# Optimization experiments

Hardware: AMD Instinct MI355X
Metric: run time of the kernel (lower is better)

Reference implementation:

```python
import jax, jax.numpy as jnp
import numpy as np

HIDDEN = 2048
NUM_HEADS = 16
NUM_KV_HEADS = 8
HEAD_DIM = 128
EPS = 1e-6
ROPE_THETA = 10000.0
T = 2048
Q_SIZE = NUM_HEADS * HEAD_DIM          # 2048
KV_SIZE = NUM_KV_HEADS * HEAD_DIM      # 1024


def setup_inputs() -> dict:
    key = jax.random.key(0)
    k1, k2, k3, k4, k5 = jax.random.split(key, 5)
    positions = jnp.arange(T, dtype=jnp.int32)
    hidden_states = jax.random.normal(k1, (T, HIDDEN), dtype=jnp.float32)
    s = 0.02
    qkv_w = jax.random.normal(k2, (Q_SIZE + 2 * KV_SIZE, HIDDEN), dtype=jnp.float32) * s
    o_w = jax.random.normal(k3, (HIDDEN, Q_SIZE), dtype=jnp.float32) * s
    q_norm_w = jnp.ones((HEAD_DIM,), dtype=jnp.float32) + 0.1 * jax.random.normal(k4, (HEAD_DIM,), dtype=jnp.float32)
    k_norm_w = jnp.ones((HEAD_DIM,), dtype=jnp.float32) + 0.1 * jax.random.normal(k5, (HEAD_DIM,), dtype=jnp.float32)
    return {"positions": positions, "hidden_states": hidden_states,
            "qkv_w": qkv_w, "q_norm_w": q_norm_w, "k_norm_w": k_norm_w, "o_w": o_w}


def _rms_norm(x, w):
    # x: [T, H, D], normalize over last dim
    var = jnp.mean(x * x, axis=-1, keepdims=True)
    return x * jax.lax.rsqrt(var + EPS) * w


def _rope(x, positions):
    # neox-style rotary over full head_dim; x: [T, H, D]
    half = HEAD_DIM // 2
    inv_freq = 1.0 / (ROPE_THETA ** (jnp.arange(0, half, dtype=jnp.float32) / half))
    freqs = positions.astype(jnp.float32)[:, None] * inv_freq  # [T, D/2]
    cos = jnp.cos(freqs)[:, None, :]  # [T, 1, D/2]
    sin = jnp.sin(freqs)[:, None, :]
    x1, x2 = x[..., :half], x[..., half:]
    return jnp.concatenate([x1 * cos - x2 * sin, x2 * cos + x1 * sin], axis=-1)


def reference(positions, hidden_states, qkv_w, q_norm_w, k_norm_w, o_w):
    G = NUM_HEADS // NUM_KV_HEADS  # query groups per kv head
    scale = HEAD_DIM ** -0.5
    qkv = hidden_states @ qkv_w.T  # [T, Q+2KV]
    q, k, v = jnp.split(qkv, [Q_SIZE, Q_SIZE + KV_SIZE], axis=-1)
    q = q.reshape(T, NUM_HEADS, HEAD_DIM)
    k = k.reshape(T, NUM_KV_HEADS, HEAD_DIM)
    v = v.reshape(T, NUM_KV_HEADS, HEAD_DIM)
    # qkv_bias=False path -> per-head RMSNorm on q and k
    q = _rms_norm(q, q_norm_w)
    k = _rms_norm(k, k_norm_w)
    q = _rope(q, positions)
    k = _rope(k, positions)
    # GQA causal attention
    qg = q.reshape(T, NUM_KV_HEADS, G, HEAD_DIM)
    scores = jnp.einsum('qkgd,skd->kgqs', qg, k) * scale  # [KV, G, T, T]
    causal = positions[:, None] >= positions[None, :]  # [T, T]
    scores = jnp.where(causal, scores, jnp.finfo(scores.dtype).min)
    probs = jax.nn.softmax(scores, axis=-1)
    ctx = jnp.einsum('kgqs,skd->qkgd', probs, v)  # [T, KV, G, D]
    ctx = ctx.reshape(T, Q_SIZE)
    return ctx @ o_w.T  # [T, HIDDEN]
```

## Files before the change

### kernel.cpp

```cpp
#include <hip/hip_runtime.h>
#include <math.h>

#define T_SEQ     2048
#define HIDDEN_   2048
#define NUM_HEADS 16
#define NUM_KV    8
#define HEAD_DIM  128
#define Q_SIZE    2048
#define KV_SIZE   1024
#define QKV_N     4096
#define QK_N      3072
#define EPS_      1e-6f

typedef __attribute__((ext_vector_type(8))) short short8;
typedef __attribute__((ext_vector_type(4))) float floatx4;

__device__ __forceinline__ unsigned short f2bf(float f) {
    unsigned int u = __float_as_uint(f);
    u += 0x7fffu + ((u >> 16) & 1u);
    return (unsigned short)(u >> 16);
}
__device__ __forceinline__ float b2f(unsigned short u) {
    return __uint_as_float((unsigned int)u << 16);
}

__device__ __forceinline__ void stage16(const unsigned short* g, unsigned short* lds_base) {
    __builtin_amdgcn_global_load_lds(
        (const __attribute__((address_space(1))) unsigned int*)g,
        (__attribute__((address_space(3))) unsigned int*)lds_base, 16, 0, 0);
}

#define H4 (T_SEQ * HIDDEN_ / 4)
#define W4 (QKV_N * HIDDEN_ / 4)
#define O4 (Q_SIZE * HIDDEN_ / 4)

__global__ __launch_bounds__(256) void convert_all(
    const float* __restrict__ hidden, const float* __restrict__ qkv_w,
    const float* __restrict__ o_w, unsigned short* __restrict__ hbf,
    unsigned short* __restrict__ wbf, unsigned short* __restrict__ obf)
{
    int i = blockIdx.x * 256 + threadIdx.x;
    const float4* src;
    ushort4* dst;
    int j;
    if (i < H4)            { src = (const float4*)hidden; dst = (ushort4*)hbf; j = i; }
    else if (i < H4 + W4)  { src = (const float4*)qkv_w;  dst = (ushort4*)wbf; j = i - H4; }
    else                   { src = (const float4*)o_w;    dst = (ushort4*)obf; j = i - H4 - W4;
                             if (j >= O4) return; }
    float4 v = src[j];
    ushort4 o;
    o.x = f2bf(v.x); o.y = f2bf(v.y); o.z = f2bf(v.z); o.w = f2bf(v.w);
    dst[j] = o;
}

template<int MODE>
__global__ __launch_bounds__(1024, 8) void gemm_nt_bf16(
    const unsigned short* __restrict__ A, const unsigned short* __restrict__ B,
    float* __restrict__ C,
    unsigned short* __restrict__ Qb, unsigned short* __restrict__ Kb,
    unsigned short* __restrict__ Vt,
    const int* __restrict__ positions,
    const float* __restrict__ qw, const float* __restrict__ kw,
    int M, int N, int K)
{
    __shared__ unsigned short smem[32768];
    unsigned short* const As0 = smem;
    unsigned short* const Bs0 = smem + 16384;

    const int tid  = threadIdx.x;
    const int w    = tid >> 6;
    const int lane = tid & 63;
    const int colL = lane & 15;
    const int quad = lane >> 4;
    const int bm = blockIdx.y * 128;
    const int bn = blockIdx.x * 128;
    const int wr = w >> 2;
    const int wc = w & 3;
    const int wm = wr * 32;
    const int wn = wc * 32;

    floatx4 acc[2][2];
    #pragma unroll
    for (int i = 0; i < 2; ++i)
        #pragma unroll
        for (int j = 0; j < 2; ++j)
            acc[i][j] = (floatx4){0.f, 0.f, 0.f, 0.f};

    const int s_r  = tid >> 3;
    const int s_lc = (tid & 7) ^ (s_r & 7);

    auto stage_tile = [&](int buf, int k0) {
        stage16(A + (size_t)(bm + s_r) * K + k0 + s_lc * 8,
                As0 + buf * 8192 + tid * 8);
        stage16(B + (size_t)(bn + s_r) * K + k0 + s_lc * 8,
                Bs0 + buf * 8192 + tid * 8);
    };

    const int nt = K >> 6;
    stage_tile(0, 0);

    for (int t = 0; t < nt; ++t) {
        const int b = t & 1;
        if (t + 1 < nt) {
            stage_tile(b ^ 1, (t + 1) << 6);
            asm volatile("s_waitcnt vmcnt(2)" ::: "memory");
        } else {
            asm volatile("s_waitcnt vmcnt(0)" ::: "memory");
        }
        __builtin_amdgcn_s_barrier();
        __builtin_amdgcn_sched_barrier(0);

        const unsigned short* la = As0 + b * 8192;
        const unsigned short* lb = Bs0 + b * 8192;
        #pragma unroll
        for (int kk = 0; kk < 2; ++kk) {
            short8 af[2], bfv[2];
            #pragma unroll
            for (int i = 0; i < 2; ++i) {
                int ra = wm + i * 16 + colL;
                af[i]  = *(const short8*)&la[ra * 64 + (((kk * 4 + quad) ^ (ra & 7)) * 8)];
            }
            #pragma unroll
            for (int j = 0; j < 2; ++j) {
                int rb = wn + j * 16 + colL;
                bfv[j] = *(const short8*)&lb[rb * 64 + (((kk * 4 + quad) ^ (rb & 7)) * 8)];
            }
            #pragma unroll
            for (int i = 0; i < 2; ++i)
                #pragma unroll
                for (int j = 0; j < 2; ++j)
                    acc[i][j] = __builtin_amdgcn_mfma_f32_16x16x32_bf16(af[i], bfv[j], acc[i][j], 0, 0, 0);
        }
        __builtin_amdgcn_sched_barrier(0);
        asm volatile("" ::: "memory");
        __builtin_amdgcn_s_barrier();
    }

    if constexpr (MODE == 0) {
        #pragma unroll
        for (int i = 0; i < 2; ++i)
            #pragma unroll
            for (int j = 0; j < 2; ++j)
                #pragma unroll
                for (int rr = 0; rr < 4; ++rr) {
                    int row = bm + wm + i * 16 + quad * 4 + rr;
                    int cc2 = bn + wn + j * 16 + colL;
                    C[(size_t)row * N + cc2] = acc[i][j][rr];
                }
    } else {
        if (bn < QK_N) {
            __shared__ float sums[4][128];
            unsigned short* xnL = smem;

            float p[2][4];
            #pragma unroll
            for (int i = 0; i < 2; ++i)
                #pragma unroll
                for (int rr = 0; rr < 4; ++rr) {
                    float sv = 0.f;
                    #pragma unroll
                    for (int j = 0; j < 2; ++j)
                        sv = fmaf(acc[i][j][rr], acc[i][j][rr], sv);
                    p[i][rr] = sv;
                }
            #pragma unroll
            for (int off = 1; off < 16; off <<= 1)
                #pragma unroll
                for (int i = 0; i < 2; ++i)
                    #pragma unroll
                    for (int rr = 0; rr < 4; ++rr)
                        p[i][rr] += __shfl_xor(p[i][rr], off, 64);
            if (colL == 0) {
                #pragma unroll
                for (int i = 0; i < 2; ++i)
                    #pragma unroll
                    for (int rr = 0; rr < 4; ++rr)
                        sums[wc][wm + i * 16 + quad * 4 + rr] = p[i][rr];
            }
            __syncthreads();

            float inv_r[2][4];
            #pragma unroll
            for (int i = 0; i < 2; ++i)
                #pragma unroll
                for (int rr = 0; rr < 4; ++rr) {
                    int row = wm + i * 16 + quad * 4 + rr;
                    float tot = (sums[0][row] + sums[1][row]) + (sums[2][row] + sums[3][row]);
                    inv_r[i][rr] = rsqrtf(tot * (1.0f / HEAD_DIM) + EPS_);
                }

            const float* nw = (bn < Q_SIZE) ? qw : kw;
            float wv[2];
            #pragma unroll
            for (int j = 0; j < 2; ++j)
                wv[j] = nw[wn + j * 16 + colL];

            #pragma unroll
            for (int i = 0; i < 2; ++i)
                #pragma unroll
                for (int j = 0; j < 2; ++j) {
                    ushort4 pk;
                    pk.x = f2bf(acc[i][j][0] * inv_r[i][0] * wv[j]);
                    pk.y = f2bf(acc[i][j][1] * inv_r[i][1] * wv[j]);
                    pk.z = f2bf(acc[i][j][2] * inv_r[i][2] * wv[j]);
                    pk.w = f2bf(acc[i][j][3] * inv_r[i][3] * wv[j]);
                    int d = wn + j * 16 + colL;
                    *(ushort4*)&xnL[d * 132 + wm + i * 16 + quad * 4] = pk;
                }
            __syncthreads();
            {
                const int r = tid >> 3;
                const int oct = tid & 7;
                const float pos = (float)positions[bm + r];
                const bool is_q = (bn < Q_SIZE);
                const float l2r = 13.287712379549449f / 64.0f;
                const float sc = 0.08838834764831845f;
                unsigned short* rowp;
                if (is_q) rowp = Qb + (size_t)(bm + r) * Q_SIZE + (bn >> 7) * HEAD_DIM;
                else      rowp = Kb + ((size_t)((bn - Q_SIZE) >> 7) * T_SEQ + bm + r) * HEAD_DIM;

                #pragma unroll
                for (int f4 = 0; f4 < 8; f4 += 4) {
                    ushort4 lo, hi;
                    #pragma unroll
                    for (int e = 0; e < 4; ++e) {
                        int f = oct * 8 + f4 + e;
                        float x1 = b2f(xnL[f * 132 + r]);
                        float x2 = b2f(xnL[(f + 64) * 132 + r]);
                        float sv, cv;
                        __sincosf(pos * exp2f(-(float)f * l2r), &sv, &cv);
                        float olo = fmaf(x1, cv, -x2 * sv);
                        float ohi = fmaf(x2, cv,  x1 * sv);
                        if (is_q) { olo *= sc; ohi *= sc; }
                        ((unsigned short*)&lo)[e] = f2bf(olo);
                        ((unsigned short*)&hi)[e] = f2bf(ohi);
                    }
                    *(ushort4*)(rowp + oct * 8 + f4)      = lo;
                    *(ushort4*)(rowp + 64 + oct * 8 + f4) = hi;
                }
            }
        } else {
            const int kvh = (bn - QK_N) >> 7;
            #pragma unroll
            for (int i = 0; i < 2; ++i)
                #pragma unroll
                for (int j = 0; j < 2; ++j) {
                    int d = wn + j * 16 + colL;
                    int tok = bm + wm + i * 16 + quad * 4;
                    ushort4 o;
                    o.x = f2bf(acc[i][j][0]); o.y = f2bf(acc[i][j][1]);
                    o.z = f2bf(acc[i][j][2]); o.w = f2bf(acc[i][j][3]);
                    *(ushort4*)&Vt[((size_t)kvh * HEAD_DIM + d) * T_SEQ + tok] = o;
                }
        }
    }
}

#define BQ 64
#define BK 32

__global__ __launch_bounds__(256) void attn_mfma(
    const unsigned short* __restrict__ Qb, const unsigned short* __restrict__ Kb,
    const unsigned short* __restrict__ Vt, unsigned short* __restrict__ ctxb,
    float* __restrict__ partO, float* __restrict__ partL)
{
    const int h = blockIdx.y;
    int qt, ch;
    {
        int x = blockIdx.x;
        if (x < 16) { qt = 16 + x; ch = 0; }
        else {
            int p = (x - 16) >> 1;
            if (((x - 16) & 1) == 0) { qt = 15 - p; ch = 0; }
            else                     { qt = 31 - p; ch = 1; }
        }
    }
    const int nch = (qt >= 16) ? 2 : 1;
    const int units = (ch == 0) ? ((qt + 1 < 16) ? 2 * (qt + 1) : 32)
                                : (2 * (qt + 1) - 32);
    const int q0 = qt * BQ;
    const int kv = h >> 1;
    const int tid = threadIdx.x;
    const int w = tid >> 6;
    const int lane = tid & 63;
    const int col = lane & 15;
    const int quad = lane >> 4;

    __shared__ unsigned short Ks[2][32 * 128];
    __shared__ unsigned short Vs[2][144 * 32];
    __shared__ unsigned short Ps[4][16][40];

    {
        int x = tid * 2;
        unsigned short vv = (x < 32) ? (unsigned short)0x3F80 : (unsigned short)0;
        ushort2 o = {vv, vv};
        *(ushort2*)&Vs[0][128 * 32 + x] = o;
        *(ushort2*)&Vs[1][128 * 32 + x] = o;
    }
    asm volatile("s_waitcnt lgkmcnt(0)" ::: "memory");

    short8 qf[4];
    {
        const unsigned short* qp = Qb + (size_t)(q0 + w * 16 + col) * Q_SIZE + h * HEAD_DIM;
        #pragma unroll
        for (int c = 0; c < 4; ++c)
            qf[c] = *(const short8*)(qp + c * 32 + quad * 8);
    }

    const unsigned short* kg[2];
    const unsigned short* vg[2];
    #pragma unroll
    for (int it = 0; it < 2; ++it) {
        int s = it * 256 + tid;
        int kr = s >> 4, kp = s & 15, kj = kp ^ (kr & 15);
        kg[it] = Kb + (size_t)kv * T_SEQ * HEAD_DIM + kr * HEAD_DIM + kj * 8;
        int vr = s >> 2, vp = s & 3, vj = vp ^ ((vr >> 1) & 3);
        vg[it] = Vt + (size_t)kv * HEAD_DIM * T_SEQ + (size_t)vr * T_SEQ + vj * 8;
    }

    floatx4 Ob[9];
    #pragma unroll
    for (int cb = 0; cb < 9; ++cb) Ob[cb] = (floatx4){0.f, 0.f, 0.f, 0.f};

    const int wave_qmin = q0 + w * 16;
    const int wave_qmax = wave_qmin + 15;
    const int tok_base = ch * 1024;

    #pragma unroll
    for (int it = 0; it < 2; ++it) {
        stage16(kg[it] + (size_t)tok_base * HEAD_DIM, &Ks[0][(it * 256 + w * 64) * 8]);
        stage16(vg[it] + tok_base, &Vs[0][(it * 256 + w * 64) * 8]);
    }

    for (int u = 0; u < units; ++u) {
        const int t0 = tok_base + u * BK;
        if (u + 1 < units) {
            const int tn = t0 + BK;
            const int b = (u + 1) & 1;
            #pragma unroll
            for (int it = 0; it < 2; ++it) {
                stage16(kg[it] + (size_t)tn * HEAD_DIM, &Ks[b][(it * 256 + w * 64) * 8]);
                stage16(vg[it] + tn, &Vs[b][(it * 256 + w * 64) * 8]);
            }
            asm volatile("s_waitcnt vmcnt(4)" ::: "memory");
        } else {
            asm volatile("s_waitcnt vmcnt(0)" ::: "memory");
        }
        __builtin_amdgcn_s_barrier();
        __builtin_amdgcn_sched_barrier(0);

        if (t0 <= wave_qmax) {
            const unsigned short* ks = Ks[u & 1];
            const unsigned short* vs = Vs[u & 1];

            floatx4 S[2];
            #pragma unroll
            for (int cb = 0; cb < 2; ++cb) {
                floatx4 a = (floatx4){0.f, 0.f, 0.f, 0.f};
                #pragma unroll
                for (int c = 0; c < 4; ++c) {
                    short8 kf = *(const short8*)&ks[((cb * 16 + col) * 16 + ((c * 4 + quad) ^ col)) * 8];
                    a = __builtin_amdgcn_mfma_f32_16x16x32_bf16(kf, qf[c], a, 0, 0, 0);
                }
                S[cb] = a;
            }

            const int qr = q0 + w * 16 + col;
            if (t0 + 31 <= wave_qmin) {
                #pragma unroll
                for (int cb = 0; cb < 2; ++cb) {
                    ushort4 pk;
                    pk.x = f2bf(__expf(S[cb][0])); pk.y = f2bf(__expf(S[cb][1]));
                    pk.z = f2bf(__expf(S[cb][2])); pk.w = f2bf(__expf(S[cb][3]));
                    *(ushort4*)&Ps[w][col][cb * 16 + quad * 4] = pk;
                }
            } else {
                #pragma unroll
                for (int cb = 0; cb < 2; ++cb) {
                    int kt = t0 + cb * 16 + quad * 4;
                    ushort4 pk;
                    pk.x = (kt + 0 <= qr) ? f2bf(__expf(S[cb][0])) : (unsigned short)0;
                    pk.y = (kt + 1 <= qr) ? f2bf(__expf(S[cb][1])) : (unsigned short)0;
                    pk.z = (kt + 2 <= qr) ? f2bf(__expf(S[cb][2])) : (unsigned short)0;
                    pk.w = (kt + 3 <= qr) ? f2bf(__expf(S[cb][3])) : (unsigned short)0;
                    *(ushort4*)&Ps[w][col][cb * 16 + quad * 4] = pk;
                }
            }

            short8 pf = *(const short8*)&Ps[w][col][quad * 8];
            #pragma unroll
            for (int cb = 0; cb < 9; ++cb) {
                int vrow = cb * 16 + col;
                short8 vf = *(const short8*)&vs[(vrow * 4 + (quad ^ ((vrow >> 1) & 3))) * 8];
                Ob[cb] = __builtin_amdgcn_mfma_f32_16x16x32_bf16(pf, vf, Ob[cb], 0, 0, 0);
            }
        }
        __builtin_amdgcn_sched_barrier(0);
        asm volatile("" ::: "memory");
        __builtin_amdgcn_s_barrier();
    }

    if (nch == 1) {
        #pragma unroll
        for (int r = 0; r < 4; ++r) {
            float l = __shfl(Ob[8][r], lane & 48);
            float rl = 1.0f / l;
            const int qrow = q0 + w * 16 + quad * 4 + r;
            #pragma unroll
            for (int cb = 0; cb < 8; ++cb)
                ctxb[(size_t)qrow * Q_SIZE + h * HEAD_DIM + cb * 16 + col] = f2bf(Ob[cb][r] * rl);
        }
    } else {
        const int slot = (h * 16 + (qt - 16)) * 2 + ch;
        float* po = partO + (size_t)slot * (BQ * HEAD_DIM);
        #pragma unroll
        for (int cb = 0; cb < 8; ++cb)
            #pragma unroll
            for (int r = 0; r < 4; ++r)
                po[(w * 16 + quad * 4 + r) * HEAD_DIM + cb * 16 + col] = Ob[cb][r];
        if (col == 0) {
            #pragma unroll
            for (int r = 0; r < 4; ++r)
                partL[slot * BQ + w * 16 + quad * 4 + r] = Ob[8][r];
        }
    }
}

__global__ __launch_bounds__(256) void combine(
    const float* __restrict__ partO, const float* __restrict__ partL,
    unsigned short* __restrict__ ctxb)
{
    const int h = blockIdx.x >> 4;
    const int qi = blockIdx.x & 15;
    const int q0 = (16 + qi) * 64;
    const int slot0 = (h * 16 + qi) * 2;
    const int tid = threadIdx.x;
    const int row = tid >> 2;
    const int seg = tid & 3;

    const float l = partL[slot0 * 64 + row] + partL[(slot0 + 1) * 64 + row];
    const float rl = 1.0f / l;
    const float* p0 = partO + (size_t)slot0 * 8192 + row * 128 + seg * 32;
    const float* p1 = p0 + 8192;
    unsigned short* dst = ctxb + (size_t)(q0 + row) * Q_SIZE + h * HEAD_DIM + seg * 32;
    #pragma unroll
    for (int m = 0; m < 8; ++m) {
        float4 a = *(const float4*)(p0 + m * 4);
        float4 b = *(const float4*)(p1 + m * 4);
        ushort4 o;
        o.x = f2bf((a.x + b.x) * rl); o.y = f2bf((a.y + b.y) * rl);
        o.z = f2bf((a.z + b.z) * rl); o.w = f2bf((a.w + b.w) * rl);
        *(ushort4*)(dst + m * 4) = o;
    }
}

extern "C" void kernel_launch(void* const* d_in, const int* in_sizes, int n_in,
                              void* d_out, int out_size, void* d_ws, size_t ws_size,
                              hipStream_t stream)
{
    const int*   positions = (const int*)d_in[0];
    const float* hidden    = (const float*)d_in[1];
    const float* qkv_w     = (const float*)d_in[2];
    const float* q_norm_w  = (const float*)d_in[3];
    const float* k_norm_w  = (const float*)d_in[4];
    const float* o_w       = (const float*)d_in[5];
    float* out = (float*)d_out;

    const size_t MB = 1024 * 1024;
    char* ws = (char*)d_ws;
    unsigned short* obf  = (unsigned short*)ws;
    unsigned short* hbf  = (unsigned short*)(ws + 8 * MB);
    unsigned short* wbf  = (unsigned short*)(ws + 16 * MB);
    unsigned short* Vt   = (unsigned short*)(ws + 32 * MB);
    unsigned short* Qb   = (unsigned short*)(ws + 36 * MB);
    unsigned short* Kb   = (unsigned short*)(ws + 44 * MB);
    unsigned short* ctxb = (unsigned short*)(ws + 48 * MB);
    float* partL         = (float*)(ws + 8 * MB);
    float* partO         = (float*)(ws + 16 * MB);

    convert_all<<<(H4 + W4 + O4 + 255) / 256, 256, 0, stream>>>(
        hidden, qkv_w, o_w, hbf, wbf, obf);
    gemm_nt_bf16<1><<<dim3(QKV_N / 128, T_SEQ / 128), 1024, 0, stream>>>(
        hbf, wbf, nullptr, Qb, Kb, Vt, positions, q_norm_w, k_norm_w,
        T_SEQ, QKV_N, HIDDEN_);
    attn_mfma<<<dim3(48, NUM_HEADS), 256, 0, stream>>>(Qb, Kb, Vt, ctxb, partO, partL);
    combine<<<256, 256, 0, stream>>>(partO, partL, ctxb);
    gemm_nt_bf16<0><<<dim3(Q_SIZE / 128, T_SEQ / 128), 1024, 0, stream>>>(
        ctxb, obf, out, nullptr, nullptr, nullptr, nullptr, nullptr, nullptr,
        T_SEQ, Q_SIZE, HIDDEN_);
}
```

Baseline: 226.0 us.

## Split attention KV range into 512-token chunks with table-driven scheduling

Attention work is split more finely: each query tile's KV range is cut into chunks of up to 512 tokens (up to 4 chunks), with a constant table ordering the work longest-first across 1280 blocks instead of 768. The combine kernel now reduces 2 to 4 partial outputs per tile. This targets load imbalance and low occupancy in causal attention, at the cost of more partial-result traffic and a larger combine pass. Partials overflow into the output buffer, which is overwritten later by the output projection.

```diff
diff --git a/kernel.cpp b/kernel.cpp
--- a/kernel.cpp
+++ b/kernel.cpp
@@ -259,25 +259,41 @@
 #define BQ 64
 #define BK 32
 
+__constant__ unsigned char WORK[80] = {
+    124,125,126,127,
+    120,121,122,  116,117,118,  112,113,114,  108,109,110,
+    104,105,106,  100,101,102,   96, 97, 98,   92, 93, 94,
+     88, 89,  84, 85,  80, 81,  76, 77,  72, 73,  68, 69,  64, 65,
+     60, 61,
+     56, 52, 48, 44, 40, 36, 32,
+     28,
+    123, 90, 57, 24,
+    119, 86, 53, 20,
+    115, 82, 49, 16,
+    111, 78, 45, 12,
+    107, 74, 41,  8,
+    103, 70, 37,  4,
+     99, 66, 33,  0
+};
+
+__device__ __forceinline__ int slot_base(int qt) {
+    return (qt < 16) ? (qt - 8) * 2
+         : (qt < 24) ? 16 + (qt - 16) * 3
+                     : 40 + (qt - 24) * 4;
+}
+
 __global__ __launch_bounds__(256) void attn_mfma(
     const unsigned short* __restrict__ Qb, const unsigned short* __restrict__ Kb,
     const unsigned short* __restrict__ Vt, unsigned short* __restrict__ ctxb,
-    float* __restrict__ partO, float* __restrict__ partL)
+    float* __restrict__ pO1, float* __restrict__ pO2, float* __restrict__ pL)
 {
-    const int h = blockIdx.y;
-    int qt, ch;
-    {
-        int x = blockIdx.x;
-        if (x < 16) { qt = 16 + x; ch = 0; }
-        else {
-            int p = (x - 16) >> 1;
-            if (((x - 16) & 1) == 0) { qt = 15 - p; ch = 0; }
-            else                     { qt = 31 - p; ch = 1; }
-        }
-    }
-    const int nch = (qt >= 16) ? 2 : 1;
-    const int units = (ch == 0) ? ((qt + 1 < 16) ? 2 * (qt + 1) : 32)
-                                : (2 * (qt + 1) - 32);
+    const int bnum = blockIdx.x;
+    const int h = bnum & 15;
+    const int enc = WORK[bnum >> 4];
+    const int qt = enc >> 2;
+    const int ch = enc & 3;
+    const int units0 = 2 * (qt + 1) - ch * 16;
+    const int units = (units0 < 16) ? units0 : 16;
     const int q0 = qt * BQ;
     const int kv = h >> 1;
     const int tid = threadIdx.x;
@@ -324,7 +340,7 @@
 
     const int wave_qmin = q0 + w * 16;
     const int wave_qmax = wave_qmin + 15;
-    const int tok_base = ch * 1024;
+    const int tok_base = ch * 512;
 
     #pragma unroll
     for (int it = 0; it < 2; ++it) {
@@ -400,7 +416,7 @@
         __builtin_amdgcn_s_barrier();
     }
 
-    if (nch == 1) {
+    if (qt < 8) {
         #pragma unroll
         for (int r = 0; r < 4; ++r) {
             float l = __shfl(Ob[8][r], lane & 48);
@@ -411,8 +427,9 @@
                 ctxb[(size_t)qrow * Q_SIZE + h * HEAD_DIM + cb * 16 + col] = f2bf(Ob[cb][r] * rl);
         }
     } else {
-        const int slot = (h * 16 + (qt - 16)) * 2 + ch;
-        float* po = partO + (size_t)slot * (BQ * HEAD_DIM);
+        const int slot = h * 72 + slot_base(qt) + ch;
+        float* po = (slot < 768) ? pO1 + (size_t)slot * (BQ * HEAD_DIM)
+                                 : pO2 + (size_t)(slot - 768) * (BQ * HEAD_DIM);
         #pragma unroll
         for (int cb = 0; cb < 8; ++cb)
             #pragma unroll
@@ -421,35 +438,49 @@
         if (col == 0) {
             #pragma unroll
             for (int r = 0; r < 4; ++r)
-                partL[slot * BQ + w * 16 + quad * 4 + r] = Ob[8][r];
+                pL[slot * BQ + w * 16 + quad * 4 + r] = Ob[8][r];
         }
     }
 }
 
 __global__ __launch_bounds__(256) void combine(
-    const float* __restrict__ partO, const float* __restrict__ partL,
-    unsigned short* __restrict__ ctxb)
+    const float* __restrict__ pO1, const float* __restrict__ pO2,
+    const float* __restrict__ pL, unsigned short* __restrict__ ctxb)
 {
-    const int h = blockIdx.x >> 4;
-    const int qi = blockIdx.x & 15;
-    const int q0 = (16 + qi) * 64;
-    const int slot0 = (h * 16 + qi) * 2;
+    const int bx = blockIdx.x;
+    const int h = bx / 24;
+    const int qt = 8 + (bx % 24);
+    const int nch = (qt < 16) ? 2 : (qt < 24) ? 3 : 4;
+    const int slot0 = h * 72 + slot_base(qt);
     const int tid = threadIdx.x;
     const int row = tid >> 2;
     const int seg = tid & 3;
 
-    const float l = partL[slot0 * 64 + row] + partL[(slot0 + 1) * 64 + row];
+    float acc[32];
+    #pragma unroll
+    for (int m = 0; m < 32; ++m) acc[m] = 0.f;
+    float l = 0.f;
+
+    for (int c = 0; c < nch; ++c) {
+        const int slot = slot0 + c;
+        const float* po = (slot < 768) ? pO1 + (size_t)slot * (BQ * HEAD_DIM)
+                                       : pO2 + (size_t)(slot - 768) * (BQ * HEAD_DIM);
+        l += pL[slot * BQ + row];
+        const float* p = po + row * HEAD_DIM + seg * 32;
+        #pragma unroll
+        for (int m = 0; m < 8; ++m) {
+            float4 a = *(const float4*)(p + m * 4);
+            acc[m * 4 + 0] += a.x; acc[m * 4 + 1] += a.y;
+            acc[m * 4 + 2] += a.z; acc[m * 4 + 3] += a.w;
+        }
+    }
     const float rl = 1.0f / l;
-    const float* p0 = partO + (size_t)slot0 * 8192 + row * 128 + seg * 32;
-    const float* p1 = p0 + 8192;
-    unsigned short* dst = ctxb + (size_t)(q0 + row) * Q_SIZE + h * HEAD_DIM + seg * 32;
+    unsigned short* dst = ctxb + (size_t)(qt * BQ + row) * Q_SIZE + h * HEAD_DIM + seg * 32;
     #pragma unroll
     for (int m = 0; m < 8; ++m) {
-        float4 a = *(const float4*)(p0 + m * 4);
-        float4 b = *(const float4*)(p1 + m * 4);
         ushort4 o;
-        o.x = f2bf((a.x + b.x) * rl); o.y = f2bf((a.y + b.y) * rl);
-        o.z = f2bf((a.z + b.z) * rl); o.w = f2bf((a.w + b.w) * rl);
+        o.x = f2bf(acc[m * 4 + 0] * rl); o.y = f2bf(acc[m * 4 + 1] * rl);
+        o.z = f2bf(acc[m * 4 + 2] * rl); o.w = f2bf(acc[m * 4 + 3] * rl);
         *(ushort4*)(dst + m * 4) = o;
     }
 }
@@ -475,16 +506,17 @@
     unsigned short* Qb   = (unsigned short*)(ws + 36 * MB);
     unsigned short* Kb   = (unsigned short*)(ws + 44 * MB);
     unsigned short* ctxb = (unsigned short*)(ws + 48 * MB);
-    float* partL         = (float*)(ws + 8 * MB);
-    float* partO         = (float*)(ws + 16 * MB);
+    float* pO1 = (float*)(ws + 8 * MB);
+    float* pO2 = out;
+    float* pL  = out + 384 * (BQ * HEAD_DIM);
 
     convert_all<<<(H4 + W4 + O4 + 255) / 256, 256, 0, stream>>>(
         hidden, qkv_w, o_w, hbf, wbf, obf);
     gemm_nt_bf16<1><<<dim3(QKV_N / 128, T_SEQ / 128), 1024, 0, stream>>>(
         hbf, wbf, nullptr, Qb, Kb, Vt, positions, q_norm_w, k_norm_w,
         T_SEQ, QKV_N, HIDDEN_);
-    attn_mfma<<<dim3(48, NUM_HEADS), 256, 0, stream>>>(Qb, Kb, Vt, ctxb, partO, partL);
-    combine<<<256, 256, 0, stream>>>(partO, partL, ctxb);
+    attn_mfma<<<1280, 256, 0, stream>>>(Qb, Kb, Vt, ctxb, pO1, pO2, pL);
+    combine<<<384, 256, 0, stream>>>(pO1, pO2, pL, ctxb);
     gemm_nt_bf16<0><<<dim3(Q_SIZE / 128, T_SEQ / 128), 1024, 0, stream>>>(
         ctxb, obf, out, nullptr, nullptr, nullptr, nullptr, nullptr, nullptr,
         T_SEQ, Q_SIZE, HIDDEN_);
```

Result: no change. 228.7 us (+1.2%).
